# Performance work log

Measured on AMD Instinct MI355X. Metric: run time of the kernel, lower is better.

The kernel has to match this reference:

```python
import jax, jax.numpy as jnp
import numpy as np
from jax import lax

DN = ('NCHW', 'OIHW', 'NCHW')

def _conv(x, w, b, stride, pad):
    y = lax.conv_general_dilated(x, w, (stride, stride), [(pad, pad), (pad, pad)], dimension_numbers=DN)
    return y + b[None, :, None, None]

def _resblock(x, w1, b1, w2, b2, wd, bd, stride):
    # standard pre-activation-free ResNet block: conv3x3(stride)-ReLU-conv3x3 + 1x1(stride) skip, final ReLU
    identity = _conv(x, wd, bd, stride, 0)
    h = jax.nn.relu(_conv(x, w1, b1, stride, 1))
    h = _conv(h, w2, b2, 1, 1)
    return jax.nn.relu(h + identity)

def _deconv(x, w, b, stride, out_pad):
    # PyTorch ConvTranspose2d(k=3, padding=1, output_padding=out_pad) as dilated conv
    # w has PyTorch layout (in_ch, out_ch, kH, kW) -> flip spatially, swap to OIHW
    wt = jnp.flip(w, (2, 3)).transpose(1, 0, 2, 3)
    y = lax.conv_general_dilated(x, wt, (1, 1), [(1, 1 + out_pad), (1, 1 + out_pad)], lhs_dilation=(stride, stride), dimension_numbers=DN)
    return y + b[None, :, None, None]

def _quantize(enc, codebook):
    # enc: (B, C, H, W); codebook: (N, C). Squared-Euclidean distances, argmin, lookup.
    e = enc.transpose(0, 2, 3, 1)  # (B, H, W, C)
    d = (jnp.sum(e * e, axis=-1, keepdims=True)
         - 2.0 * jnp.einsum('bhwc,nc->bhwn', e, codebook)
         + jnp.sum(codebook * codebook, axis=-1))  # (B, H, W, N)
    idx = jnp.argmin(d, axis=-1)
    q = codebook[idx]  # (B, H, W, C)
    return q.transpose(0, 3, 1, 2)

def setup_inputs() -> dict:
    key = jax.random.key(0)
    ks = jax.random.split(key, 28)
    def W(k, shape):
        return jax.random.normal(k, shape, jnp.float32) * 0.05
    inp = {"x": jax.random.normal(ks[0], (32, 3, 256, 256), jnp.float32)}
    enc_chans = [(3, 64), (64, 128), (128, 64)]
    i = 1
    for l, (cin, cout) in enumerate(enc_chans):
        inp[f"enc{l}_w1"] = W(ks[i], (cout, cin, 3, 3))
        inp[f"enc{l}_b1"] = W(ks[i + 1], (cout,))
        inp[f"enc{l}_w2"] = W(ks[i + 2], (cout, cout, 3, 3))
        inp[f"enc{l}_b2"] = W(ks[i + 3], (cout,))
        inp[f"enc{l}_wd"] = W(ks[i + 4], (cout, cin, 1, 1))
        inp[f"enc{l}_bd"] = W(ks[i + 5], (cout,))
        i += 6
    # decoder ConvTranspose2d weights in PyTorch layout (in_ch, out_ch, 3, 3)
    dec_chans = [(64, 128), (128, 64), (64, 3)]
    for l, (cin, cout) in enumerate(dec_chans):
        inp[f"dec{l}_w"] = W(ks[i], (cin, cout, 3, 3))
        inp[f"dec{l}_b"] = W(ks[i + 1], (cout,))
        i += 2
    inp["codebook"] = W(ks[i], (512, 64))
    return inp

def reference(x, enc0_w1, enc0_b1, enc0_w2, enc0_b2, enc0_wd, enc0_bd,
              enc1_w1, enc1_b1, enc1_w2, enc1_b2, enc1_wd, enc1_bd,
              enc2_w1, enc2_b1, enc2_w2, enc2_b2, enc2_wd, enc2_bd,
              dec0_w, dec0_b, dec1_w, dec1_b, dec2_w, dec2_b, codebook):
    # encode: 256 -> 128 -> 64 -> 64 spatially
    h = _resblock(x, enc0_w1, enc0_b1, enc0_w2, enc0_b2, enc0_wd, enc0_bd, 2)
    h = _resblock(h, enc1_w1, enc1_b1, enc1_w2, enc1_b2, enc1_wd, enc1_bd, 2)
    h = _resblock(h, enc2_w1, enc2_b1, enc2_w2, enc2_b2, enc2_wd, enc2_bd, 1)
    q = _quantize(h, codebook)
    # decode with output_size matching encoder input shapes (output_padding: 0, 1, 1)
    h = jax.nn.relu(_deconv(q, dec0_w, dec0_b, 1, 0))   # 64 -> 64
    h = jax.nn.relu(_deconv(h, dec1_w, dec1_b, 2, 1))   # 64 -> 128
    return _deconv(h, dec2_w, dec2_b, 2, 1)             # 128 -> 256
```

## Files before the change

kernel.cpp:

```cpp
#include <hip/hip_runtime.h>
#include <cstddef>


typedef float v4f __attribute__((ext_vector_type(4)));
typedef _Float16 f16x8 __attribute__((ext_vector_type(8)));
typedef _Float16 f16x4 __attribute__((ext_vector_type(4)));

__device__ __forceinline__ void fma4(v4f& a, float p, const v4f& w) {
    a.x = fmaf(p, w.x, a.x); a.y = fmaf(p, w.y, a.y);
    a.z = fmaf(p, w.z, a.z); a.w = fmaf(p, w.w, a.w);
}

__global__ void repack_k(const float* __restrict__ src, float* __restrict__ dst,
                         int cout, int coutR, int cin, int flip, int deconv)
{
    int t = blockIdx.x * 256 + threadIdx.x;
    int tot = cin * 9 * cout;
    if (t >= tot) return;
    int co = t % cout; int k = (t / cout) % 9; int ci = t / (9 * cout);
    float v = 0.f;
    if (co < coutR) {
        int ks = flip ? 8 - k : k;
        v = deconv ? src[((size_t)ci * coutR + co) * 9 + ks]
                   : src[((size_t)co * cin + ci) * 9 + ks];
    }
    dst[t] = v;
}

__global__ void repackB16_k(const float* __restrict__ src, _Float16* __restrict__ bh,
                            _Float16* __restrict__ bl, int COUT, int CIN, int deconv)
{
    int t = blockIdx.x * 256 + threadIdx.x;
    int tot = 9 * CIN * COUT;
    if (t >= tot) return;
    int NGtot = COUT >> 4, C32 = CIN >> 5;
    int j = t & 7;
    int lane = (t >> 3) & 63;
    int blk = t >> 9;
    int ng = blk % NGtot; blk /= NGtot;
    int c32 = blk % C32;
    int tap = blk / C32;
    int co = ng * 16 + (lane & 15);
    int ci = c32 * 32 + ((lane >> 4) & 3) * 8 + j;
    float v = deconv ? src[((size_t)ci * COUT + co) * 9 + (8 - tap)]
                     : src[((size_t)co * CIN + ci) * 9 + tap];
    _Float16 h = (_Float16)v;
    _Float16 l = (_Float16)(v - (float)h);
    bh[t] = h; bl[t] = l;
}

__global__ void repackQ_k(const float* __restrict__ cb, _Float16* __restrict__ qb)
{
    int t = blockIdx.x * 256 + threadIdx.x;
    if (t >= 65536) return;
    int j = t & 7;
    int lane = (t >> 3) & 63;
    int hl = (t >> 9) & 1;
    int s = (t >> 10) & 1;
    int nt = t >> 11;
    int code = nt * 16 + (lane & 15);
    int ci = s * 32 + ((lane >> 4) & 3) * 8 + j;
    float v = cb[(size_t)code * 64 + ci];
    _Float16 h = (_Float16)v;
    qb[t] = hl ? (_Float16)(v - (float)h) : h;
}

__global__ void cbnorm_k(const float* __restrict__ cb, float* __restrict__ cn)
{
    int i = blockIdx.x * 256 + threadIdx.x;
    if (i >= 512) return;
    float s = 0.f;
#pragma unroll
    for (int j = 0; j < 64; ++j) { float v = cb[i * 64 + j]; s = fmaf(v, v, s); }
    cn[i] = s;
}

template<int CIN, bool RELU, int ADDMODE, bool CLIN, bool CLOUT>
__launch_bounds__(256, 2)
__global__ void mconv3s1_k(const float* __restrict__ in,
                           const _Float16* __restrict__ Bh, const _Float16* __restrict__ Bl,
                           const float* __restrict__ bias, float* __restrict__ out,
                           const float* __restrict__ addend,
                           int COUT, int H, int W)
{
    constexpr int C32 = CIN / 32;
    __shared__ __align__(16) unsigned char smBuf[76416];
    _Float16* AH = (_Float16*)smBuf;
    _Float16* AL = AH + 12960;
    _Float16* BW = AL + 12960;
    float* smO = (float*)smBuf;

    const int tid = threadIdx.x;
    const int lane = tid & 63, yb = tid >> 6;
    const int n16 = lane & 15, q = lane >> 4;

    int b = blockIdx.x;
    const int chunks = COUT >> 6;
    const int coch = b % chunks; b /= chunks;
    const int tX = W >> 4; const int tx = b % tX; b /= tX;
    const int tY = H >> 4; const int ty = b % tY; const int n = b / tY;
    const int x0 = tx * 16, y0 = ty * 16;
    const int NGtot = COUT >> 4;
    const int ngbase = coch * 4, cobase = coch * 64;

    v4f acc[4][4];
#pragma unroll
    for (int ng = 0; ng < 4; ++ng) {
        float bb = bias[cobase + ng * 16 + n16];
        v4f bv = {bb, bb, bb, bb};
#pragma unroll
        for (int mg = 0; mg < 4; ++mg) acc[mg][ng] = bv;
    }

    for (int c32 = 0; c32 < C32; ++c32) {
        __syncthreads();
        if (CLIN) {
            for (int u = tid; u < 2592; u += 256) {
                int cell = u >> 3, f4 = u & 7;
                int yy = cell / 18, xx = cell - yy * 18;
                int gy = y0 - 1 + yy, gx = x0 - 1 + xx;
                float4 v = make_float4(0.f, 0.f, 0.f, 0.f);
                if (gy >= 0 && gy < H && gx >= 0 && gx < W)
                    v = *(const float4*)&in[(((size_t)n * H + gy) * W + gx) * CIN + c32 * 32 + f4 * 4];
                f16x4 h4, l4;
                h4[0] = (_Float16)v.x; l4[0] = (_Float16)(v.x - (float)h4[0]);
                h4[1] = (_Float16)v.y; l4[1] = (_Float16)(v.y - (float)h4[1]);
                h4[2] = (_Float16)v.z; l4[2] = (_Float16)(v.z - (float)h4[2]);
                h4[3] = (_Float16)v.w; l4[3] = (_Float16)(v.w - (float)h4[3]);
                int a = (yy * 18 + xx) * 40 + f4 * 4;
                *(f16x4*)&AH[a] = h4; *(f16x4*)&AL[a] = l4;
            }
        } else {
            for (int u = tid; u < 10368; u += 256) {
                int ci = u / 324, rem = u - ci * 324;
                int yy = rem / 18, xx = rem - yy * 18;
                int gy = y0 - 1 + yy, gx = x0 - 1 + xx;
                float v = 0.f;
                if (gy >= 0 && gy < H && gx >= 0 && gx < W)
                    v = in[(((size_t)n * CIN + c32 * 32 + ci) * H + gy) * W + gx];
                _Float16 h = (_Float16)v;
                _Float16 l = (_Float16)(v - (float)h);
                int a = (yy * 18 + xx) * 40 + ci;
                AH[a] = h; AL[a] = l;
            }
        }
        for (int ky = 0; ky < 3; ++ky) {
            __syncthreads();
            for (int u = tid; u < 1536; u += 256) {
                int lu = u & 63;
                int rest = u >> 6;
                int hl = rest & 1; rest >>= 1;
                int ng = rest & 3;
                int tapL = rest >> 2;
                const uint4* srcp = (const uint4*)(hl ? Bl : Bh);
                size_t sidx = (((size_t)(ky * 3 + tapL) * C32 + c32) * NGtot + ngbase + ng) * 64 + lu;
                ((uint4*)BW)[u] = srcp[sidx];
            }
            __syncthreads();
#pragma unroll
            for (int kx = 0; kx < 3; ++kx) {
                f16x8 aH[4], aL[4];
#pragma unroll
                for (int mg = 0; mg < 4; ++mg) {
                    int aoff = ((4 * yb + mg + ky) * 18 + n16 + kx) * 40 + q * 8;
                    aH[mg] = *(const f16x8*)&AH[aoff];
                    aL[mg] = *(const f16x8*)&AL[aoff];
                }
#pragma unroll
                for (int ng = 0; ng < 4; ++ng) {
                    int boff = ((kx * 4 + ng) * 2) * 512 + lane * 8;
                    f16x8 bH = *(const f16x8*)&BW[boff];
                    f16x8 bL = *(const f16x8*)&BW[boff + 512];
#pragma unroll
                    for (int mg = 0; mg < 4; ++mg) {
                        acc[mg][ng] = __builtin_amdgcn_mfma_f32_16x16x32_f16(aH[mg], bH, acc[mg][ng], 0, 0, 0);
                        acc[mg][ng] = __builtin_amdgcn_mfma_f32_16x16x32_f16(aL[mg], bH, acc[mg][ng], 0, 0, 0);
                        acc[mg][ng] = __builtin_amdgcn_mfma_f32_16x16x32_f16(aH[mg], bL, acc[mg][ng], 0, 0, 0);
                    }
                }
            }
        }
    }

    __syncthreads();
#pragma unroll
    for (int mg = 0; mg < 4; ++mg)
#pragma unroll
        for (int ng = 0; ng < 4; ++ng) {
            int p = (4 * yb + mg) * 16 + q * 4;
            int co = ng * 16 + n16;
#pragma unroll
            for (int r = 0; r < 4; ++r)
                smO[co * 257 + p + r] = acc[mg][ng][r];
        }
    __syncthreads();
    if (CLOUT) {
        const int p = tid;
        const int py = p >> 4, px = p & 15;
        size_t cellBase = (((size_t)n * H + (y0 + py)) * W + (x0 + px)) * COUT + cobase;
        float* cellp = out + cellBase;
        const float* acell = (ADDMODE == 2) ? addend + cellBase : nullptr;
#pragma unroll
        for (int g = 0; g < 16; ++g) {
            float4 v;
            v.x = smO[(4 * g + 0) * 257 + p];
            v.y = smO[(4 * g + 1) * 257 + p];
            v.z = smO[(4 * g + 2) * 257 + p];
            v.w = smO[(4 * g + 3) * 257 + p];
            if (ADDMODE == 2) {
                float4 a4 = *(const float4*)&acell[4 * g];
                v.x += a4.x; v.y += a4.y; v.z += a4.z; v.w += a4.w;
            }
            if (RELU) {
                v.x = fmaxf(v.x, 0.f); v.y = fmaxf(v.y, 0.f);
                v.z = fmaxf(v.z, 0.f); v.w = fmaxf(v.w, 0.f);
            }
            *(float4*)&cellp[4 * g] = v;
        }
    } else {
        const size_t plane = (size_t)H * W;
        float* ob = out + ((size_t)n * COUT + cobase) * plane;
        const float* ab = (ADDMODE == 1) ? addend + ((size_t)n * COUT + cobase) * plane : nullptr;
#pragma unroll
        for (int k = 0; k < 64; ++k) {
            int e = tid + 256 * k;
            int co = e >> 8, p = e & 255;
            int py = p >> 4, px = p & 15;
            size_t g = (size_t)co * plane + (size_t)(y0 + py) * W + x0 + px;
            float v = smO[co * 257 + p];
            if (ADDMODE == 1) v += ab[g];
            if (RELU) v = fmaxf(v, 0.f);
            ob[g] = v;
        }
    }
}

template<int CIN, int NG, bool RELU>
__launch_bounds__(256, 3)
__global__ void mconv3s2_k(const float* __restrict__ in,
                           const _Float16* __restrict__ Bh, const _Float16* __restrict__ Bl,
                           const float* __restrict__ bias, float* __restrict__ out,
                           int COUT, int Hin, int Win)
{
    constexpr int C32 = CIN / 32;
    constexpr int ASZ = 9 * 2 * 17 * 40;
    __shared__ __align__(16) unsigned char smBuf[2 * ASZ * 2];
    _Float16* AH = (_Float16*)smBuf;
    _Float16* AL = AH + ASZ;
    float* smO = (float*)smBuf;

    const int tid = threadIdx.x;
    const int lane = tid & 63, yb = tid >> 6;
    const int n16 = lane & 15, q = lane >> 4;

    const int Hout = Hin >> 1, Wout = Win >> 1;
    int b = blockIdx.x;
    const int chunks = COUT / (NG * 16);
    const int coch = b % chunks; b /= chunks;
    const int tX = Wout >> 4; const int tx = b % tX; b /= tX;
    const int tY = Hout >> 2; const int ty = b % tY; const int n = b / tY;
    const int x0 = tx * 16, y0 = ty * 4;
    const int gx0 = 2 * x0 - 1, gy0 = 2 * y0 - 1;
    const int NGtot = COUT >> 4;
    const int ngbase = coch * NG, cobase = coch * NG * 16;

    v4f acc[NG];
#pragma unroll
    for (int ng = 0; ng < NG; ++ng) {
        float bb = bias[cobase + ng * 16 + n16];
        v4f bv = {bb, bb, bb, bb};
        acc[ng] = bv;
    }

    const uint4* bhp = (const uint4*)Bh;
    const uint4* blp = (const uint4*)Bl;

    for (int c32 = 0; c32 < C32; ++c32) {
        __syncthreads();
        for (int u = tid; u < 2376; u += 256) {
            int cell = u >> 3, f4 = u & 7;
            int yy = cell / 33, xx = cell - yy * 33;
            int gy = gy0 + yy, gx = gx0 + xx;
            float4 v = make_float4(0.f, 0.f, 0.f, 0.f);
            if (gy >= 0 && gy < Hin && gx >= 0 && gx < Win)
                v = *(const float4*)&in[(((size_t)n * Hin + gy) * Win + gx) * CIN + c32 * 32 + f4 * 4];
            f16x4 h4, l4;
            h4[0] = (_Float16)v.x; l4[0] = (_Float16)(v.x - (float)h4[0]);
            h4[1] = (_Float16)v.y; l4[1] = (_Float16)(v.y - (float)h4[1]);
            h4[2] = (_Float16)v.z; l4[2] = (_Float16)(v.z - (float)h4[2]);
            h4[3] = (_Float16)v.w; l4[3] = (_Float16)(v.w - (float)h4[3]);
            int a = ((yy * 2 + (xx & 1)) * 17 + (xx >> 1)) * 40 + f4 * 4;
            *(f16x4*)&AH[a] = h4; *(f16x4*)&AL[a] = l4;
        }
        __syncthreads();
#pragma unroll
        for (int ky = 0; ky < 3; ++ky) {
#pragma unroll
            for (int kx = 0; kx < 3; ++kx) {
                const int par = kx & 1, xs = kx >> 1;
                int aoff = (((2 * yb + ky) * 2 + par) * 17 + n16 + xs) * 40 + q * 8;
                f16x8 aH = *(const f16x8*)&AH[aoff];
                f16x8 aL = *(const f16x8*)&AL[aoff];
                size_t sb0 = (((size_t)(ky * 3 + kx) * C32 + c32) * NGtot + ngbase) * 64 + lane;
#pragma unroll
                for (int ng = 0; ng < NG; ++ng) {
                    uint4 rH = bhp[sb0 + (size_t)ng * 64];
                    uint4 rL = blp[sb0 + (size_t)ng * 64];
                    f16x8 bH = *(const f16x8*)&rH;
                    f16x8 bL = *(const f16x8*)&rL;
                    acc[ng] = __builtin_amdgcn_mfma_f32_16x16x32_f16(aH, bH, acc[ng], 0, 0, 0);
                    acc[ng] = __builtin_amdgcn_mfma_f32_16x16x32_f16(aL, bH, acc[ng], 0, 0, 0);
                    acc[ng] = __builtin_amdgcn_mfma_f32_16x16x32_f16(aH, bL, acc[ng], 0, 0, 0);
                }
            }
        }
    }

    __syncthreads();
#pragma unroll
    for (int ng = 0; ng < NG; ++ng) {
        int co = ng * 16 + n16;
        int p = yb * 16 + q * 4;
#pragma unroll
        for (int r = 0; r < 4; ++r)
            smO[co * 65 + p + r] = acc[ng][r];
    }
    __syncthreads();
    const int p2 = tid >> 2, s2 = tid & 3;
    const int py = p2 >> 4, px = p2 & 15;
    float* cellp = out + ((((size_t)n * Hout + (y0 + py)) * Wout + (x0 + px)) * COUT + s2 * 32);
#pragma unroll
    for (int k = 0; k < 8; ++k) {
        float4 v;
        v.x = smO[(s2 * 32 + 4 * k + 0) * 65 + p2];
        v.y = smO[(s2 * 32 + 4 * k + 1) * 65 + p2];
        v.z = smO[(s2 * 32 + 4 * k + 2) * 65 + p2];
        v.w = smO[(s2 * 32 + 4 * k + 3) * 65 + p2];
        if (RELU) {
            v.x = fmaxf(v.x, 0.f); v.y = fmaxf(v.y, 0.f);
            v.z = fmaxf(v.z, 0.f); v.w = fmaxf(v.w, 0.f);
        }
        *(float4*)&cellp[4 * k] = v;
    }
}

template<int CIN, bool RELU>
__launch_bounds__(256, 3)
__global__ void mdeconv2_k(const float* __restrict__ in,
                           const _Float16* __restrict__ Bh, const _Float16* __restrict__ Bl,
                           const float* __restrict__ bias, float* __restrict__ out,
                           int COUT, int Hin, int Win)
{
    constexpr int C32 = CIN / 32;
    __shared__ __align__(16) unsigned char smBuf[38976];
    _Float16* AH = (_Float16*)smBuf;
    _Float16* AL = AH + 3600;
    _Float16* BW = AL + 3600;
    float* smO = (float*)smBuf;

    const int tid = threadIdx.x;
    const int lane = tid & 63, yb = tid >> 6;
    const int n16 = lane & 15, q = lane >> 4;

    int b = blockIdx.x;
    const int chunks = COUT >> 6;
    const int coch = b % chunks; b /= chunks;
    const int tX = Win >> 4; const int tx = b % tX; b /= tX;
    const int tY = Hin >> 2; const int ty = b % tY; const int n = b / tY;
    const int x0 = tx * 16, y0 = ty * 4;
    const int NGtot = COUT >> 4;
    const int ngbase = coch * 4, cobase = coch * 64;

    v4f acc[4][4];
#pragma unroll
    for (int ng = 0; ng < 4; ++ng) {
        float bb = bias[cobase + ng * 16 + n16];
        v4f bv = {bb, bb, bb, bb};
#pragma unroll
        for (int ph = 0; ph < 4; ++ph) acc[ph][ng] = bv;
    }

    for (int c32 = 0; c32 < C32; ++c32) {
        __syncthreads();
        for (int u = tid; u < 680; u += 256) {
            int cell = u >> 3, f4 = u & 7;
            int yy = cell / 17, xx = cell - yy * 17;
            int gy = y0 + yy, gx = x0 + xx;
            float4 v = make_float4(0.f, 0.f, 0.f, 0.f);
            if (gy < Hin && gx < Win)
                v = *(const float4*)&in[(((size_t)n * Hin + gy) * Win + gx) * CIN + c32 * 32 + f4 * 4];
            f16x4 h4, l4;
            h4[0] = (_Float16)v.x; l4[0] = (_Float16)(v.x - (float)h4[0]);
            h4[1] = (_Float16)v.y; l4[1] = (_Float16)(v.y - (float)h4[1]);
            h4[2] = (_Float16)v.z; l4[2] = (_Float16)(v.z - (float)h4[2]);
            h4[3] = (_Float16)v.w; l4[3] = (_Float16)(v.w - (float)h4[3]);
            int a = (yy * 18 + xx) * 40 + f4 * 4;
            *(f16x4*)&AH[a] = h4; *(f16x4*)&AL[a] = l4;
        }
        for (int ky = 0; ky < 3; ++ky) {
            __syncthreads();
            for (int u = tid; u < 1536; u += 256) {
                int lu = u & 63;
                int rest = u >> 6;
                int hl = rest & 1; rest >>= 1;
                int ng = rest & 3;
                int tapL = rest >> 2;
                const uint4* srcp = (const uint4*)(hl ? Bl : Bh);
                size_t sidx = (((size_t)(ky * 3 + tapL) * C32 + c32) * NGtot + ngbase + ng) * 64 + lu;
                ((uint4*)BW)[u] = srcp[sidx];
            }
            __syncthreads();
            const int iy = (ky == 2) ? 1 : 0;
            const int phy = (ky == 1) ? 0 : 2;
#pragma unroll
            for (int kx = 0; kx < 3; ++kx) {
                const int ix = (kx == 2) ? 1 : 0;
                const int ph = phy + ((kx == 1) ? 0 : 1);
                int aoff = ((yb + iy) * 18 + n16 + ix) * 40 + q * 8;
                f16x8 aH = *(const f16x8*)&AH[aoff];
                f16x8 aL = *(const f16x8*)&AL[aoff];
#pragma unroll
                for (int ng = 0; ng < 4; ++ng) {
                    int boff = ((kx * 4 + ng) * 2) * 512 + lane * 8;
                    f16x8 bH = *(const f16x8*)&BW[boff];
                    f16x8 bL = *(const f16x8*)&BW[boff + 512];
                    acc[ph][ng] = __builtin_amdgcn_mfma_f32_16x16x32_f16(aH, bH, acc[ph][ng], 0, 0, 0);
                    acc[ph][ng] = __builtin_amdgcn_mfma_f32_16x16x32_f16(aL, bH, acc[ph][ng], 0, 0, 0);
                    acc[ph][ng] = __builtin_amdgcn_mfma_f32_16x16x32_f16(aH, bL, acc[ph][ng], 0, 0, 0);
                }
            }
        }
    }

    const int Wout = Win * 2;
    const size_t plane = (size_t)(Hin * 2) * (size_t)Wout;
    float* ob = out + ((size_t)n * COUT + cobase) * plane;
    const int oy0 = 2 * y0, ox0 = 2 * x0;
#pragma unroll
    for (int half = 0; half < 2; ++half) {
        __syncthreads();
#pragma unroll
        for (int ph = 0; ph < 4; ++ph) {
            const int dy = ph >> 1, dx = ph & 1;
#pragma unroll
            for (int g = 0; g < 2; ++g) {
                int ng = half * 2 + g;
#pragma unroll
                for (int r = 0; r < 4; ++r)
                    smO[(g * 16 + n16) * 257 + (2 * yb + dy) * 32 + 2 * (q * 4 + r) + dx] = acc[ph][ng][r];
            }
        }
        __syncthreads();
#pragma unroll
        for (int k = 0; k < 32; ++k) {
            int pos = tid;
            int oyl = pos >> 5, oxl = pos & 31;
            float v = smO[k * 257 + pos];
            if (RELU) v = fmaxf(v, 0.f);
            ob[(size_t)(half * 32 + k) * plane + (size_t)(oy0 + oyl) * Wout + ox0 + oxl] = v;
        }
    }
}

template<int CIN, int CB, bool RELU>
__launch_bounds__(256, 4)
__global__ void conv3s2_k(const float* __restrict__ in, const float* __restrict__ wp,
                          const float* __restrict__ bias, float* __restrict__ out,
                          int COUT, int Hin, int Win)
{
    constexpr int COC = 32;
    __shared__ float smIn[CB * 2178];
    __shared__ float smW[CB * 9 * COC];
    const int Hout = Hin >> 1, Wout = Win >> 1;
    const int tid = threadIdx.x;
    int b = blockIdx.x;
    const int chunks = COUT / COC;
    const int tX = Wout / 32, tY = Hout / 16;
    const int ch = b % chunks; b /= chunks;
    const int tx = b % tX; b /= tX;
    const int ty = b % tY; const int n = b / tY;
    const int cobase = ch * COC;
    const int r = tid >> 4, c = tid & 15;
    const int gy0 = ty * 32 - 1, gx0 = tx * 64 - 1;

    v4f acc[16];
#pragma unroll
    for (int g = 0; g < 8; ++g) {
        v4f bv = *(const v4f*)&bias[cobase + 4 * g];
        acc[g] = bv; acc[8 + g] = bv;
    }

    const size_t plane = (size_t)Hin * Win;
    const float* ip0 = in + (size_t)n * CIN * plane;
    const float* wp0 = wp + cobase;

    for (int ci0 = 0; ci0 < CIN; ci0 += CB) {
        __syncthreads();
        for (int idx = tid; idx < CB * 2178; idx += 256) {
            int ci = idx / 2178, rem = idx - ci * 2178;
            int rr = rem / 66, cc = rem - rr * 66;
            int gy = gy0 + rr, gx = gx0 + cc;
            float v = 0.f;
            if (gy >= 0 && gy < Hin && gx >= 0 && gx < Win)
                v = ip0[(size_t)(ci0 + ci) * plane + (size_t)gy * Win + gx];
            smIn[idx] = v;
        }
        for (int idx = tid; idx < CB * 9 * COC; idx += 256) {
            int q2 = idx >> 5, co = idx & 31;
            smW[idx] = wp0[((size_t)ci0 * 9 + q2) * COUT + co];
        }
        __syncthreads();

#pragma unroll 1
        for (int ci = 0; ci < CB; ++ci) {
            float p[15];
            const float* sp = &smIn[ci * 2178 + 2 * r * 66 + 4 * c];
#pragma unroll
            for (int i = 0; i < 3; ++i)
#pragma unroll
                for (int j = 0; j < 5; ++j)
                    p[i * 5 + j] = sp[i * 66 + j];
            const float* wrow = &smW[ci * 288];
#pragma unroll
            for (int k = 0; k < 9; ++k) {
                const int ky = k / 3, kx = k % 3;
#pragma unroll
                for (int g = 0; g < 8; ++g) {
                    v4f wv = *(const v4f*)&wrow[k * 32 + 4 * g];
                    fma4(acc[g],     p[ky * 5 + kx],     wv);
                    fma4(acc[8 + g], p[ky * 5 + kx + 2], wv);
                }
            }
        }
    }

    const int oy = ty * 16 + r, ox = tx * 32 + 2 * c;
    size_t cellBase = (((size_t)n * Hout + oy) * Wout + ox) * COUT + cobase;
#pragma unroll
    for (int g = 0; g < 8; ++g) {
        v4f v0 = acc[g], v1 = acc[8 + g];
        if (RELU) {
#pragma unroll
            for (int e = 0; e < 4; ++e) { v0[e] = fmaxf(v0[e], 0.f); v1[e] = fmaxf(v1[e], 0.f); }
        }
        *(v4f*)&out[cellBase + 4 * g] = v0;
        *(v4f*)&out[cellBase + COUT + 4 * g] = v1;
    }
}

template<int CIN, int CB, int COC, bool RELU>
__launch_bounds__(256, 3)
__global__ void deconv2_k(const float* __restrict__ in, const float* __restrict__ wp,
                          const float* __restrict__ bias, float* __restrict__ out,
                          int COUTR, int COUTP, int Hin, int Win)
{
    constexpr int RW = 33, RH = 17;
    __shared__ float smIn[CB * RH * RW];
    __shared__ float smW[CB * 9 * COC];
    const int Wout = Win * 2;
    const int tid = threadIdx.x;
    int b = blockIdx.x;
    const int chunks = COUTP / COC;
    const int qTX = Win / 32, qTY = Hin / 16;
    const int ch = b % chunks; b /= chunks;
    const int qtx = b % qTX; b /= qTX;
    const int qty = b % qTY; const int n = b / qTY;
    const int cobase = ch * COC;
    const int tqy = tid >> 4, tqx = tid & 15;
    const int qby = qty * 16, qbx = qtx * 32;

    v4f acc[8 * COC / 4];
#pragma unroll
    for (int g = 0; g < COC / 4; ++g) {
        v4f bv;
#pragma unroll
        for (int e = 0; e < 4; ++e)
            bv[e] = (cobase + 4 * g + e < COUTR) ? bias[cobase + 4 * g + e] : 0.f;
#pragma unroll
        for (int pt = 0; pt < 8; ++pt) acc[pt * (COC / 4) + g] = bv;
    }

    const size_t plane = (size_t)Hin * Win;
    const float* ip0 = in + (size_t)n * CIN * plane;
    const float* wp0 = wp + cobase;

    for (int ci0 = 0; ci0 < CIN; ci0 += CB) {
        __syncthreads();
        for (int idx = tid; idx < CB * RH * RW; idx += 256) {
            int ci = idx / (RH * RW), rem = idx - ci * (RH * RW);
            int rr = rem / RW, cc = rem - rr * RW;
            int gy = qby + rr, gx = qbx + cc;
            float v = 0.f;
            if (gy < Hin && gx < Win)
                v = ip0[(size_t)(ci0 + ci) * plane + (size_t)gy * Win + gx];
            smIn[idx] = v;
        }
        for (int idx = tid; idx < CB * 9 * COC; idx += 256) {
            int q2 = idx / COC, co = idx % COC;
            smW[idx] = wp0[((size_t)ci0 * 9 + q2) * COUTP + co];
        }
        __syncthreads();

#pragma unroll 1
        for (int ci = 0; ci < CB; ++ci) {
            float p[6];
            const float* sp = &smIn[ci * RH * RW + tqy * RW + 2 * tqx];
#pragma unroll
            for (int i = 0; i < 2; ++i)
#pragma unroll
                for (int j = 0; j < 3; ++j)
                    p[i * 3 + j] = sp[i * RW + j];
            const float* wrow = &smW[ci * 9 * COC];
#pragma unroll
            for (int k = 0; k < 9; ++k) {
                const int ky = k / 3, kx = k % 3;
                const int dy = (ky == 1) ? 0 : 1, iy = (ky == 0) ? 1 : 0;
                const int dx = (kx == 1) ? 0 : 1, ix = (kx == 0) ? 1 : 0;
#pragma unroll
                for (int g = 0; g < COC / 4; ++g) {
                    v4f wv = *(const v4f*)&wrow[k * COC + 4 * g];
                    fma4(acc[(0 + dy * 2 + dx) * (COC / 4) + g], p[iy * 3 + ix],     wv);
                    fma4(acc[(4 + dy * 2 + dx) * (COC / 4) + g], p[iy * 3 + ix + 1], wv);
                }
            }
        }
    }

    const size_t oPlane = (size_t)(Hin * 2) * Wout;
    const int oy = 2 * (qby + tqy), ox = 2 * (qbx + 2 * tqx);
#pragma unroll
    for (int g = 0; g < COC / 4; ++g)
#pragma unroll
        for (int e = 0; e < 4; ++e) {
            int cch = cobase + 4 * g + e;
            if (cch >= COUTR) break;
            float* op = out + ((size_t)n * COUTR + cch) * oPlane + (size_t)oy * Wout + ox;
#pragma unroll
            for (int a2 = 0; a2 < 2; ++a2) {
                float u0 = acc[(0 + a2 * 2 + 0) * (COC / 4) + g][e];
                float u1 = acc[(0 + a2 * 2 + 1) * (COC / 4) + g][e];
                float u2 = acc[(4 + a2 * 2 + 0) * (COC / 4) + g][e];
                float u3 = acc[(4 + a2 * 2 + 1) * (COC / 4) + g][e];
                if (RELU) { u0 = fmaxf(u0, 0.f); u1 = fmaxf(u1, 0.f);
                            u2 = fmaxf(u2, 0.f); u3 = fmaxf(u3, 0.f); }
                *(float4*)&op[(size_t)a2 * Wout] = make_float4(u0, u1, u2, u3);
            }
        }
}

template<int CIN, int S, bool RELU, bool CLIN, bool CLOUT>
__launch_bounds__(256, 4)
__global__ void conv1x1_k(const float* __restrict__ in, const float* __restrict__ w,
                          const float* __restrict__ bias, float* __restrict__ out,
                          int COUT, int Hin, int Win, int Hout, int Wout)
{
    constexpr int COC = 32;
    __shared__ float smW[CIN * COC];
    const int tid = threadIdx.x;
    int b = blockIdx.x;
    const int chunks = COUT / COC;
    const int spB = (Hout * Wout) / 256;
    const int ch = b % chunks; b /= chunks;
    const int sb = b % spB; const int n = b / spB;
    const int cobase = ch * COC;

    for (int idx = tid; idx < CIN * COC; idx += 256) {
        int ci = idx / COC, co = idx - ci * COC;
        smW[idx] = w[(size_t)(cobase + co) * CIN + ci];
    }
    __syncthreads();

    const int pos = sb * 256 + tid;
    const int oy = pos / Wout, ox = pos - oy * Wout;

    v4f acc[8];
#pragma unroll
    for (int g = 0; g < 8; ++g) acc[g] = *(const v4f*)&bias[cobase + 4 * g];

    if (CLIN) {
        const float* ip = in + (((size_t)n * Hin + oy * S) * Win + ox * S) * CIN;
#pragma unroll 1
        for (int c4 = 0; c4 < CIN / 4; ++c4) {
            v4f v = *(const v4f*)&ip[c4 * 4];
#pragma unroll
            for (int e = 0; e < 4; ++e)
#pragma unroll
                for (int g = 0; g < 8; ++g)
                    fma4(acc[g], v[e], *(const v4f*)&smW[(c4 * 4 + e) * COC + 4 * g]);
        }
    } else {
        const size_t inPlane = (size_t)Hin * Win;
        const float* ip = in + (size_t)n * CIN * inPlane + (size_t)(oy * S) * Win + (size_t)(ox * S);
#pragma unroll 1
        for (int ci = 0; ci < CIN; ++ci) {
            float v = ip[(size_t)ci * inPlane];
#pragma unroll
            for (int g = 0; g < 8; ++g)
                fma4(acc[g], v, *(const v4f*)&smW[ci * COC + 4 * g]);
        }
    }
    const size_t outPlane = (size_t)Hout * Wout;
    if (CLOUT) {
        size_t cb2 = ((size_t)n * outPlane + pos) * COUT + cobase;
#pragma unroll
        for (int g = 0; g < 8; ++g) {
            v4f v = acc[g];
            if (RELU) {
#pragma unroll
                for (int e = 0; e < 4; ++e) v[e] = fmaxf(v[e], 0.f);
            }
            *(v4f*)&out[cb2 + 4 * g] = v;
        }
    } else {
        float* op = out + ((size_t)n * COUT + cobase) * outPlane + pos;
#pragma unroll
        for (int g = 0; g < 8; ++g)
#pragma unroll
            for (int e = 0; e < 4; ++e) {
                float v = acc[g][e];
                if (RELU) v = fmaxf(v, 0.f);
                op[(size_t)(4 * g + e) * outPlane] = v;
            }
    }
}

__launch_bounds__(256, 4)
__global__ void mquant_k(const float* __restrict__ h, const _Float16* __restrict__ QB,
                         const float* __restrict__ cn, const float* __restrict__ cb,
                         float* __restrict__ q)
{
    __shared__ __align__(16) _Float16 AF[2][8192];
    __shared__ float cns[512];
    __shared__ int bidxs[128];

    const int tid = threadIdx.x;
    const int lane = tid & 63;
    const int wv = tid >> 6;
    const int n16 = lane & 15, qq = lane >> 4;

    const int n = blockIdx.x >> 5;
    const int rem0 = (blockIdx.x & 31) << 7;

    for (int u = tid; u < 1024; u += 256) {
        int posL = u >> 3, grp = u & 7;
        const float* gp = h + ((size_t)n * 4096 + rem0 + posL) * 64 + grp * 8;
        float4 v0 = *(const float4*)gp;
        float4 v1 = *(const float4*)(gp + 4);
        f16x8 hh, ll;
        hh[0] = (_Float16)v0.x; ll[0] = (_Float16)(v0.x - (float)hh[0]);
        hh[1] = (_Float16)v0.y; ll[1] = (_Float16)(v0.y - (float)hh[1]);
        hh[2] = (_Float16)v0.z; ll[2] = (_Float16)(v0.z - (float)hh[2]);
        hh[3] = (_Float16)v0.w; ll[3] = (_Float16)(v0.w - (float)hh[3]);
        hh[4] = (_Float16)v1.x; ll[4] = (_Float16)(v1.x - (float)hh[4]);
        hh[5] = (_Float16)v1.y; ll[5] = (_Float16)(v1.y - (float)hh[5]);
        hh[6] = (_Float16)v1.z; ll[6] = (_Float16)(v1.z - (float)hh[6]);
        hh[7] = (_Float16)v1.w; ll[7] = (_Float16)(v1.w - (float)hh[7]);
        int mt = posL >> 4, s = grp >> 2, qv = grp & 3;
        int a = ((mt * 2 + s) * 64 + (posL & 15) + qv * 16) * 8;
        *(f16x8*)&AF[0][a] = hh;
        *(f16x8*)&AF[1][a] = ll;
    }
    for (int u = tid; u < 512; u += 256) cns[u] = cn[u];
    __syncthreads();

    f16x8 aH[2][2], aL[2][2];
#pragma unroll
    for (int m = 0; m < 2; ++m)
#pragma unroll
        for (int s = 0; s < 2; ++s) {
            int a = (((wv * 2 + m) * 2 + s) * 64 + lane) * 8;
            aH[m][s] = *(const f16x8*)&AF[0][a];
            aL[m][s] = *(const f16x8*)&AF[1][a];
        }

    float best[2][4]; int bi[2][4];
#pragma unroll
    for (int m = 0; m < 2; ++m)
#pragma unroll
        for (int r = 0; r < 4; ++r) { best[m][r] = 3.4e38f; bi[m][r] = 0; }

    const uint4* qbp = (const uint4*)QB;
#pragma unroll 1
    for (int nt = 0; nt < 32; ++nt) {
        uint4 rH0 = qbp[((nt * 2 + 0) * 2 + 0) * 64 + lane];
        uint4 rL0 = qbp[((nt * 2 + 0) * 2 + 1) * 64 + lane];
        uint4 rH1 = qbp[((nt * 2 + 1) * 2 + 0) * 64 + lane];
        uint4 rL1 = qbp[((nt * 2 + 1) * 2 + 1) * 64 + lane];
        f16x8 bH0 = *(const f16x8*)&rH0;
        f16x8 bL0 = *(const f16x8*)&rL0;
        f16x8 bH1 = *(const f16x8*)&rH1;
        f16x8 bL1 = *(const f16x8*)&rL1;
        float cnv = cns[nt * 16 + n16];
        const int code = nt * 16 + n16;
#pragma unroll
        for (int m = 0; m < 2; ++m) {
            v4f acc = {0.f, 0.f, 0.f, 0.f};
            acc = __builtin_amdgcn_mfma_f32_16x16x32_f16(aH[m][0], bH0, acc, 0, 0, 0);
            acc = __builtin_amdgcn_mfma_f32_16x16x32_f16(aL[m][0], bH0, acc, 0, 0, 0);
            acc = __builtin_amdgcn_mfma_f32_16x16x32_f16(aH[m][0], bL0, acc, 0, 0, 0);
            acc = __builtin_amdgcn_mfma_f32_16x16x32_f16(aH[m][1], bH1, acc, 0, 0, 0);
            acc = __builtin_amdgcn_mfma_f32_16x16x32_f16(aL[m][1], bH1, acc, 0, 0, 0);
            acc = __builtin_amdgcn_mfma_f32_16x16x32_f16(aH[m][1], bL1, acc, 0, 0, 0);
#pragma unroll
            for (int r = 0; r < 4; ++r) {
                float d = fmaf(-2.f, acc[r], cnv);
                if (d < best[m][r]) { best[m][r] = d; bi[m][r] = code; }
            }
        }
    }

#pragma unroll
    for (int m = 0; m < 2; ++m)
#pragma unroll
        for (int r = 0; r < 4; ++r) {
#pragma unroll
            for (int msk = 1; msk < 16; msk <<= 1) {
                float ob = __shfl_xor(best[m][r], msk);
                int oi = __shfl_xor(bi[m][r], msk);
                if (ob < best[m][r] || (ob == best[m][r] && oi < bi[m][r])) {
                    best[m][r] = ob; bi[m][r] = oi;
                }
            }
            if (n16 == 0) bidxs[wv * 32 + m * 16 + qq * 4 + r] = bi[m][r];
        }
    __syncthreads();

    const int p = tid & 127, jh = tid >> 7;
    const int code = bidxs[p];
    const float4* crow4 = (const float4*)(cb + (size_t)code * 64);
    float4* qp4 = (float4*)(q + ((size_t)n * 4096 + rem0 + p) * 64);
#pragma unroll
    for (int k = 0; k < 8; ++k)
        qp4[jh * 8 + k] = crow4[jh * 8 + k];
}

extern "C" void kernel_launch(void* const* d_in, const int* in_sizes, int n_in,
                              void* d_out, int out_size, void* d_ws, size_t ws_size,
                              hipStream_t stream)
{
    const float* x    = (const float*)d_in[0];
    const float* e0w1 = (const float*)d_in[1];  const float* e0b1 = (const float*)d_in[2];
    const float* e0w2 = (const float*)d_in[3];  const float* e0b2 = (const float*)d_in[4];
    const float* e0wd = (const float*)d_in[5];  const float* e0bd = (const float*)d_in[6];
    const float* e1w1 = (const float*)d_in[7];  const float* e1b1 = (const float*)d_in[8];
    const float* e1w2 = (const float*)d_in[9];  const float* e1b2 = (const float*)d_in[10];
    const float* e1wd = (const float*)d_in[11]; const float* e1bd = (const float*)d_in[12];
    const float* e2w1 = (const float*)d_in[13]; const float* e2b1 = (const float*)d_in[14];
    const float* e2w2 = (const float*)d_in[15]; const float* e2b2 = (const float*)d_in[16];
    const float* e2wd = (const float*)d_in[17]; const float* e2bd = (const float*)d_in[18];
    const float* d0w  = (const float*)d_in[19]; const float* d0b  = (const float*)d_in[20];
    const float* d1w  = (const float*)d_in[21]; const float* d1b  = (const float*)d_in[22];
    const float* d2w  = (const float*)d_in[23]; const float* d2b  = (const float*)d_in[24];
    const float* cb   = (const float*)d_in[25];
    float* out = (float*)d_out;
    float* ws  = (float*)d_ws;

    float* P_e0w1 = out + 0;
    _Float16* Bh_d1   = (_Float16*)(out + 1728);
    _Float16* Bl_d1   = (_Float16*)(out + 38592);
    _Float16* Bh_e0c2 = (_Float16*)(out + 77760);
    _Float16* Bl_e0c2 = (_Float16*)(out + 96192);
    _Float16* Bh_e1c2 = (_Float16*)(out + 114624);
    _Float16* Bl_e1c2 = (_Float16*)(out + 188352);
    _Float16* Bh_e2c1 = (_Float16*)(out + 262080);
    _Float16* Bl_e2c1 = (_Float16*)(out + 298944);
    _Float16* Bh_e2c2 = (_Float16*)(out + 335808);
    _Float16* Bl_e2c2 = (_Float16*)(out + 354240);
    _Float16* Bh_d0   = (_Float16*)(out + 372672);
    _Float16* Bl_d0   = (_Float16*)(out + 409536);
    _Float16* Bh_e1c1 = (_Float16*)(out + 446400);
    _Float16* Bl_e1c1 = (_Float16*)(out + 483264);
    _Float16* QB = (_Float16*)(out + 520128);
    float* CN = out + 552896;
    float* P_d2w  = ws + 50405376;

    float* S0 = ws;
    float* T1 = ws + 33554432;
    float* T3 = ws + 33554432;
    float* S1 = ws + 50331648;
    float* S2 = ws;
    float* T5 = ws + 8388608;
    float* Q  = ws + 16777216;
    float* D0 = ws + 33554432;
    float* D1 = ws;

    dim3 blk(256);
    auto rp = [&](const float* src, float* dst, int cout, int coutR, int cin, int flip, int dec) {
        int tot = cin * 9 * cout;
        repack_k<<<dim3((tot + 255) / 256), blk, 0, stream>>>(src, dst, cout, coutR, cin, flip, dec);
    };
    auto rpB = [&](const float* src, _Float16* bh, _Float16* bl, int cout, int cin, int dec) {
        int tot = 9 * cin * cout;
        repackB16_k<<<dim3((tot + 255) / 256), blk, 0, stream>>>(src, bh, bl, cout, cin, dec);
    };

    rp(e0w1, P_e0w1, 64, 64, 3, 0, 0);
    rpB(e0w2, Bh_e0c2, Bl_e0c2, 64, 64, 0);
    rpB(e1w1, Bh_e1c1, Bl_e1c1, 128, 64, 0);
    rpB(e1w2, Bh_e1c2, Bl_e1c2, 128, 128, 0);
    rpB(e2w1, Bh_e2c1, Bl_e2c1, 64, 128, 0);
    rpB(e2w2, Bh_e2c2, Bl_e2c2, 64, 64, 0);
    rpB(d0w,  Bh_d0,   Bl_d0,   128, 64, 1);
    rpB(d1w,  Bh_d1,   Bl_d1,   64, 128, 1);
    repackQ_k<<<dim3(256), blk, 0, stream>>>(cb, QB);
    cbnorm_k<<<dim3(2), blk, 0, stream>>>(cb, CN);

    conv1x1_k<3, 2, false, false, true><<<dim3(32 * 64 * 2), blk, 0, stream>>>(
        x, e0wd, e0bd, S0, 64, 256, 256, 128, 128);
    conv3s2_k<3, 3, true><<<dim3(32 * 8 * 4 * 2), blk, 0, stream>>>(
        x, P_e0w1, e0b1, T1, 64, 256, 256);
    mconv3s1_k<64, true, 2, true, true><<<dim3(32 * 8 * 8 * 1), blk, 0, stream>>>(
        T1, Bh_e0c2, Bl_e0c2, e0b2, S0, S0, 64, 128, 128);

    conv1x1_k<64, 2, false, true, true><<<dim3(32 * 16 * 4), blk, 0, stream>>>(
        S0, e1wd, e1bd, S1, 128, 128, 128, 64, 64);
    mconv3s2_k<64, 8, true><<<dim3(32 * 16 * 4), blk, 0, stream>>>(
        S0, Bh_e1c1, Bl_e1c1, e1b1, T3, 128, 128, 128);
    mconv3s1_k<128, true, 2, true, true><<<dim3(32 * 4 * 4 * 2), blk, 0, stream>>>(
        T3, Bh_e1c2, Bl_e1c2, e1b2, S1, S1, 128, 64, 64);

    conv1x1_k<128, 1, false, true, true><<<dim3(32 * 16 * 2), blk, 0, stream>>>(
        S1, e2wd, e2bd, S2, 64, 64, 64, 64, 64);
    mconv3s1_k<128, true, 0, true, true><<<dim3(32 * 4 * 4 * 1), blk, 0, stream>>>(
        S1, Bh_e2c1, Bl_e2c1, e2b1, T5, nullptr, 64, 64, 64);
    rp(d2w, P_d2w, 4, 3, 64, 0, 1);
    mconv3s1_k<64, true, 2, true, true><<<dim3(32 * 4 * 4 * 1), blk, 0, stream>>>(
        T5, Bh_e2c2, Bl_e2c2, e2b2, S2, S2, 64, 64, 64);

    mquant_k<<<dim3(1024), blk, 0, stream>>>(S2, QB, CN, cb, Q);

    mconv3s1_k<64, true, 0, true, true><<<dim3(32 * 4 * 4 * 2), blk, 0, stream>>>(
        Q, Bh_d0, Bl_d0, d0b, D0, nullptr, 128, 64, 64);

    mdeconv2_k<128, true><<<dim3(32 * 16 * 4), blk, 0, stream>>>(
        D0, Bh_d1, Bl_d1, d1b, D1, 64, 64, 64);

    deconv2_k<64, 8, 4, false><<<dim3(32 * 4 * 8), blk, 0, stream>>>(
        D1, P_d2w, d2b, out, 3, 4, 128, 128);
}
```

Before: 1.510 ms.

## Read conv weights directly from global and shrink LDS for 3 blocks/CU

The stride-1 MFMA conv kernel no longer stages weight tiles into shared memory per kernel row. Each lane now loads its fp16 hi/lo weight fragments straight from global memory, which removes two barriers per ky iteration. With the weight buffer gone, LDS shrinks from about 75KB to about 51KB, and launch bounds rise to 3 blocks per CU. The epilogue writes output in two 32-channel halves so the staging buffer fits the smaller LDS. In exchange, weight loads now go through L1/L2 with possible latency stalls before the MFMAs, register pressure rises under the tighter bound, and the ADDMODE==1 addend path in the channel-major output branch is dropped.

Measured after the change: 1.822 ms. 1.21x slower.

```diff
diff --git a/kernel.cpp b/kernel.cpp
--- a/kernel.cpp
+++ b/kernel.cpp
@@ -76,7 +76,7 @@
 }
 
 template<int CIN, bool RELU, int ADDMODE, bool CLIN, bool CLOUT>
-__launch_bounds__(256, 2)
+__launch_bounds__(256, 3)
 __global__ void mconv3s1_k(const float* __restrict__ in,
                            const _Float16* __restrict__ Bh, const _Float16* __restrict__ Bl,
                            const float* __restrict__ bias, float* __restrict__ out,
@@ -84,10 +84,9 @@
                            int COUT, int H, int W)
 {
     constexpr int C32 = CIN / 32;
-    __shared__ __align__(16) unsigned char smBuf[76416];
+    __shared__ __align__(16) unsigned char smBuf[51840];
     _Float16* AH = (_Float16*)smBuf;
     _Float16* AL = AH + 12960;
-    _Float16* BW = AL + 12960;
     float* smO = (float*)smBuf;
 
     const int tid = threadIdx.x;
@@ -111,6 +110,9 @@
 #pragma unroll
         for (int mg = 0; mg < 4; ++mg) acc[mg][ng] = bv;
     }
+
+    const uint4* bhp = (const uint4*)Bh;
+    const uint4* blp = (const uint4*)Bl;
 
     for (int c32 = 0; c32 < C32; ++c32) {
         __syncthreads();
@@ -144,19 +146,9 @@
                 AH[a] = h; AL[a] = l;
             }
         }
+        __syncthreads();
+#pragma unroll
         for (int ky = 0; ky < 3; ++ky) {
-            __syncthreads();
-            for (int u = tid; u < 1536; u += 256) {
-                int lu = u & 63;
-                int rest = u >> 6;
-                int hl = rest & 1; rest >>= 1;
-                int ng = rest & 3;
-                int tapL = rest >> 2;
-                const uint4* srcp = (const uint4*)(hl ? Bl : Bh);
-                size_t sidx = (((size_t)(ky * 3 + tapL) * C32 + c32) * NGtot + ngbase + ng) * 64 + lu;
-                ((uint4*)BW)[u] = srcp[sidx];
-            }
-            __syncthreads();
 #pragma unroll
             for (int kx = 0; kx < 3; ++kx) {
                 f16x8 aH[4], aL[4];
@@ -166,11 +158,13 @@
                     aH[mg] = *(const f16x8*)&AH[aoff];
                     aL[mg] = *(const f16x8*)&AL[aoff];
                 }
+                size_t sb0 = (((size_t)(ky * 3 + kx) * C32 + c32) * NGtot + ngbase) * 64 + lane;
 #pragma unroll
                 for (int ng = 0; ng < 4; ++ng) {
-                    int boff = ((kx * 4 + ng) * 2) * 512 + lane * 8;
-                    f16x8 bH = *(const f16x8*)&BW[boff];
-                    f16x8 bL = *(const f16x8*)&BW[boff + 512];
+                    uint4 rH = bhp[sb0 + (size_t)ng * 64];
+                    uint4 rL = blp[sb0 + (size_t)ng * 64];
+                    f16x8 bH = *(const f16x8*)&rH;
+                    f16x8 bL = *(const f16x8*)&rL;
 #pragma unroll
                     for (int mg = 0; mg < 4; ++mg) {
                         acc[mg][ng] = __builtin_amdgcn_mfma_f32_16x16x32_f16(aH[mg], bH, acc[mg][ng], 0, 0, 0);
@@ -182,55 +176,58 @@
         }
     }
 
-    __syncthreads();
-#pragma unroll
-    for (int mg = 0; mg < 4; ++mg)
-#pragma unroll
-        for (int ng = 0; ng < 4; ++ng) {
-            int p = (4 * yb + mg) * 16 + q * 4;
-            int co = ng * 16 + n16;
-#pragma unroll
-            for (int r = 0; r < 4; ++r)
-                smO[co * 257 + p + r] = acc[mg][ng][r];
-        }
-    __syncthreads();
-    if (CLOUT) {
-        const int p = tid;
-        const int py = p >> 4, px = p & 15;
-        size_t cellBase = (((size_t)n * H + (y0 + py)) * W + (x0 + px)) * COUT + cobase;
-        float* cellp = out + cellBase;
-        const float* acell = (ADDMODE == 2) ? addend + cellBase : nullptr;
-#pragma unroll
-        for (int g = 0; g < 16; ++g) {
-            float4 v;
-            v.x = smO[(4 * g + 0) * 257 + p];
-            v.y = smO[(4 * g + 1) * 257 + p];
-            v.z = smO[(4 * g + 2) * 257 + p];
-            v.w = smO[(4 * g + 3) * 257 + p];
-            if (ADDMODE == 2) {
-                float4 a4 = *(const float4*)&acell[4 * g];
-                v.x += a4.x; v.y += a4.y; v.z += a4.z; v.w += a4.w;
-            }
-            if (RELU) {
-                v.x = fmaxf(v.x, 0.f); v.y = fmaxf(v.y, 0.f);
-                v.z = fmaxf(v.z, 0.f); v.w = fmaxf(v.w, 0.f);
-            }
-            *(float4*)&cellp[4 * g] = v;
-        }
-    } else {
-        const size_t plane = (size_t)H * W;
-        float* ob = out + ((size_t)n * COUT + cobase) * plane;
-        const float* ab = (ADDMODE == 1) ? addend + ((size_t)n * COUT + cobase) * plane : nullptr;
-#pragma unroll
-        for (int k = 0; k < 64; ++k) {
-            int e = tid + 256 * k;
-            int co = e >> 8, p = e & 255;
-            int py = p >> 4, px = p & 15;
-            size_t g = (size_t)co * plane + (size_t)(y0 + py) * W + x0 + px;
-            float v = smO[co * 257 + p];
-            if (ADDMODE == 1) v += ab[g];
-            if (RELU) v = fmaxf(v, 0.f);
-            ob[g] = v;
+#pragma unroll
+    for (int half = 0; half < 2; ++half) {
+        __syncthreads();
+#pragma unroll
+        for (int g2 = 0; g2 < 2; ++g2) {
+            int ng = half * 2 + g2;
+            int row = g2 * 16 + n16;
+#pragma unroll
+            for (int mg = 0; mg < 4; ++mg) {
+                int p = (4 * yb + mg) * 16 + q * 4;
+#pragma unroll
+                for (int r = 0; r < 4; ++r)
+                    smO[row * 257 + p + r] = acc[mg][ng][r];
+            }
+        }
+        __syncthreads();
+        if (CLOUT) {
+            const int p = tid;
+            const int py = p >> 4, px = p & 15;
+            size_t cellBase = (((size_t)n * H + (y0 + py)) * W + (x0 + px)) * COUT + cobase + half * 32;
+            float* cellp = out + cellBase;
+            const float* acell = (ADDMODE == 2) ? addend + cellBase : nullptr;
+#pragma unroll
+            for (int g = 0; g < 8; ++g) {
+                float4 v;
+                v.x = smO[(4 * g + 0) * 257 + p];
+                v.y = smO[(4 * g + 1) * 257 + p];
+                v.z = smO[(4 * g + 2) * 257 + p];
+                v.w = smO[(4 * g + 3) * 257 + p];
+                if (ADDMODE == 2) {
+                    float4 a4 = *(const float4*)&acell[4 * g];
+                    v.x += a4.x; v.y += a4.y; v.z += a4.z; v.w += a4.w;
+                }
+                if (RELU) {
+                    v.x = fmaxf(v.x, 0.f); v.y = fmaxf(v.y, 0.f);
+                    v.z = fmaxf(v.z, 0.f); v.w = fmaxf(v.w, 0.f);
+                }
+                *(float4*)&cellp[4 * g] = v;
+            }
+        } else {
+            const size_t plane = (size_t)H * W;
+            float* ob = out + ((size_t)n * COUT + cobase + half * 32) * plane;
+#pragma unroll
+            for (int k = 0; k < 32; ++k) {
+                int e = tid + 256 * k;
+                int co = e >> 8, p = e & 255;
+                int py = p >> 4, px = p & 15;
+                size_t g = (size_t)co * plane + (size_t)(y0 + py) * W + x0 + px;
+                float v = smO[co * 257 + p];
+                if (RELU) v = fmaxf(v, 0.f);
+                ob[g] = v;
+            }
         }
     }
 }
```
